# Kernel tuning notes

Measured on AMD Instinct MI355X. Metric: run time of the kernel, lower is better.

Reference implementation:

```python
import jax, jax.numpy as jnp
import numpy as np

VOCAB, ENC, EMB, DEC, ATT = 10000, 2048, 512, 512, 512
B, P, S = 64, 196, 20
PAD_ID = 0


def setup_inputs() -> dict:
    key = jax.random.key(0)
    ks = jax.random.split(key, 20)
    sc = lambda *sh: 1.0 / np.sqrt(sh[-1])
    def lin(k, out, inp):
        kw, kb = jax.random.split(k)
        s = 1.0 / np.sqrt(inp)
        return (jax.random.uniform(kw, (out, inp), jnp.float32, -s, s),
                jax.random.uniform(kb, (out,), jnp.float32, -s, s))
    wenc_w, wenc_b = lin(ks[0], ATT, ENC)
    wdec_w, wdec_b = lin(ks[1], ATT, DEC)
    V_w, V_b = lin(ks[2], 1, ATT)
    h0_w, h0_b = lin(ks[3], DEC, ENC)
    c0_w, c0_b = lin(ks[4], DEC, ENC)
    W_ih, b_ih = lin(ks[5], 4 * DEC, ENC + EMB)
    W_hh, b_hh = lin(ks[6], 4 * DEC, DEC)
    fc_w, fc_b = lin(ks[7], VOCAB, DEC)
    embed_w = jax.random.normal(ks[8], (VOCAB, EMB), jnp.float32)
    embed_w = embed_w.at[PAD_ID].set(0.0)  # padding_idx row is zero
    image_feat = jax.random.normal(ks[9], (B, P, ENC), jnp.float32)
    captions_ids = jax.random.randint(ks[10], (B, S), 0, VOCAB)
    return dict(image_feat=image_feat, captions_ids=captions_ids,
                wenc_w=wenc_w, wenc_b=wenc_b, wdec_w=wdec_w, wdec_b=wdec_b,
                V_w=V_w, V_b=V_b, embed_w=embed_w,
                h0_w=h0_w, h0_b=h0_b, c0_w=c0_w, c0_b=c0_b,
                W_ih=W_ih, b_ih=b_ih, W_hh=W_hh, b_hh=b_hh,
                fc_w=fc_w, fc_b=fc_b)


def reference(image_feat, captions_ids, wenc_w, wenc_b, wdec_w, wdec_b,
              V_w, V_b, embed_w, h0_w, h0_b, c0_w, c0_b,
              W_ih, b_ih, W_hh, b_hh, fc_w, fc_b):
    # eval mode: no input noise, dropout = identity
    avg = image_feat.mean(axis=1)                                   # [B, ENC]
    h = jax.nn.relu(avg @ h0_w.T + h0_b)                            # [B, DEC]
    c = jax.nn.relu(avg @ c0_w.T + c0_b)
    enc_proj = jnp.einsum('bpe,ae->bpa', image_feat, wenc_w) + wenc_b  # [B,P,ATT]
    emb_seq = embed_w[captions_ids]                                 # [B,S,EMB]
    emb_seq = jnp.transpose(emb_seq, (1, 0, 2))                     # [S,B,EMB]

    def step(carry, emb_t):
        h, c = carry
        att = jnp.tanh(enc_proj + (h @ wdec_w.T + wdec_b)[:, None, :])  # [B,P,ATT]
        e = jnp.einsum('bpa,a->bp', att, V_w[0]) + V_b[0]               # [B,P]
        w = jax.nn.softmax(e, axis=1)
        ctx = jnp.einsum('bp,bpe->be', w, image_feat)                   # [B,ENC]
        x = jnp.concatenate([ctx, emb_t], axis=1)                       # [B,ENC+EMB]
        gates = x @ W_ih.T + b_ih + h @ W_hh.T + b_hh                   # [B,4*DEC]
        i, f, g, o = jnp.split(gates, 4, axis=1)
        c_new = jax.nn.sigmoid(f) * c + jax.nn.sigmoid(i) * jnp.tanh(g)
        h_new = jax.nn.sigmoid(o) * jnp.tanh(c_new)
        logits = h_new @ fc_w.T + fc_b                                  # [B,VOCAB]
        return (h_new, c_new), logits

    _, preds = jax.lax.scan(step, (h, c), emb_seq)                  # [S,B,VOCAB]
    return jnp.transpose(preds, (1, 0, 2))                          # [B,S,VOCAB]
```

## Files before the change

kernel.cpp:

```cpp
#include <hip/hip_runtime.h>
#include <hip/hip_bf16.h>

#define DEV static __device__ __forceinline__

typedef short s16x8 __attribute__((ext_vector_type(8)));
typedef float f32x4 __attribute__((ext_vector_type(4)));
typedef unsigned short u16;

constexpr int Bn = 64, Pn = 196, ENCn = 2048, EMBn = 512, DECn = 512, ATTn = 512;
constexpr int VOCABn = 10000, Sn = 20;

DEV u16 f2bf(float x) {
  union { float f; unsigned u; } v; v.f = x;
  unsigned r = v.u + 0x7fffu + ((v.u >> 16) & 1u);
  return (u16)(r >> 16);
}
DEV float bf2f(u16 b) {
  union { unsigned u; float f; } v; v.u = ((unsigned)b) << 16;
  return v.f;
}
DEV float sigm(float x) { return 1.f / (1.f + __expf(-x)); }
DEV float tanh_fast(float x) {
  float e = __expf(2.f * x);
  return 1.f - 2.f / (e + 1.f);
}

DEV s16x8 ld8(const u16* p) { return *reinterpret_cast<const s16x8*>(p); }
DEV f32x4 mfma(s16x8 a, s16x8 b, f32x4 c) {
  return __builtin_amdgcn_mfma_f32_16x16x32_bf16(a, b, c, 0, 0, 0);
}

#define GLOAD_LDS16(gsrc, ldst)                                                \
  __builtin_amdgcn_global_load_lds(                                            \
      (const __attribute__((address_space(1))) void*)(gsrc),                   \
      (__attribute__((address_space(3))) void*)(ldst), 16, 0, 0)

__global__ __launch_bounds__(256) void k_cvtfeat_part(
    const float* __restrict__ feat, u16* __restrict__ featbf,
    float* __restrict__ pavg) {
  int b = blockIdx.y, px = blockIdx.x;
  int d8 = threadIdx.x * 8;
  const float* p = feat + ((size_t)b * Pn + px * 7) * ENCn + d8;
  u16* q = featbf + ((size_t)b * Pn + px * 7) * ENCn + d8;
  float acc[8] = {};
#pragma unroll
  for (int k = 0; k < 7; k++) {
    float4 v0 = *(const float4*)(p + (size_t)k * ENCn);
    float4 v1 = *(const float4*)(p + (size_t)k * ENCn + 4);
    acc[0] += v0.x; acc[1] += v0.y; acc[2] += v0.z; acc[3] += v0.w;
    acc[4] += v1.x; acc[5] += v1.y; acc[6] += v1.z; acc[7] += v1.w;
    s16x8 o;
    o[0] = (short)f2bf(v0.x); o[1] = (short)f2bf(v0.y);
    o[2] = (short)f2bf(v0.z); o[3] = (short)f2bf(v0.w);
    o[4] = (short)f2bf(v1.x); o[5] = (short)f2bf(v1.y);
    o[6] = (short)f2bf(v1.z); o[7] = (short)f2bf(v1.w);
    *(s16x8*)(q + (size_t)k * ENCn) = o;
  }
  float* pp = pavg + ((size_t)px * Bn + b) * ENCn + d8;
  *(f32x4*)pp = f32x4{acc[0], acc[1], acc[2], acc[3]};
  *(f32x4*)(pp + 4) = f32x4{acc[4], acc[5], acc[6], acc[7]};
}

__global__ __launch_bounds__(256) void k_avg_final(
    const float* __restrict__ pavg, float* __restrict__ avg) {
  int idx = blockIdx.x * 256 + threadIdx.x;
  int b = idx >> 9, e4 = (idx & 511) * 4;
  float4 s = {0.f, 0.f, 0.f, 0.f};
#pragma unroll
  for (int px = 0; px < 28; px++) {
    float4 v = *(const float4*)(pavg + ((size_t)px * Bn + b) * ENCn + e4);
    s.x += v.x; s.y += v.y; s.z += v.z; s.w += v.w;
  }
  float4 o = { s.x * (1.f/196.f), s.y * (1.f/196.f), s.z * (1.f/196.f), s.w * (1.f/196.f) };
  *(float4*)(avg + (size_t)b * ENCn + e4) = o;
}

__global__ void k_cvt_all(const float* __restrict__ s0, u16* __restrict__ d0,
                          const float* __restrict__ s1, u16* __restrict__ d1,
                          const float* __restrict__ s2, u16* __restrict__ d2,
                          const float* __restrict__ s3, u16* __restrict__ d3,
                          const float* __restrict__ s4, u16* __restrict__ d4,
                          const float* __restrict__ s5, u16* __restrict__ d5,
                          u16* __restrict__ wdecT) {
  int gid = blockIdx.x * 256 + threadIdx.x, stride = gridDim.x * 256;
  auto run = [&](const float* __restrict__ s, u16* __restrict__ d, int n8) {
    for (int i = gid; i < n8; i += stride) {
      const float4* sp = (const float4*)(s + (size_t)i * 8);
      float4 a = sp[0], b = sp[1];
      s16x8 o;
      o[0] = (short)f2bf(a.x); o[1] = (short)f2bf(a.y);
      o[2] = (short)f2bf(a.z); o[3] = (short)f2bf(a.w);
      o[4] = (short)f2bf(b.x); o[5] = (short)f2bf(b.y);
      o[6] = (short)f2bf(b.z); o[7] = (short)f2bf(b.w);
      *(s16x8*)(d + (size_t)i * 8) = o;
    }
  };
  run(s0, d0, 131072);
  run(s1, d1, 32768);
  run(s2, d2, 655360);
  run(s3, d3, 131072);
  run(s4, d4, 640000);
  run(s5, d5, 640000);
  for (int i = gid; i < 262144; i += stride) {
    int n = i >> 9, k = i & 511;
    wdecT[(size_t)k * 512 + n] = f2bf(s1[i]);
  }
}

__global__ __launch_bounds__(256) void k_h0c0(
    const float* __restrict__ avg,
    const float* __restrict__ h0w, const float* __restrict__ h0b,
    const float* __restrict__ c0w, const float* __restrict__ c0b,
    u16* __restrict__ h0out, float* __restrict__ c0out,
    float* __restrict__ decpart) {
  int idx = blockIdx.x * 256 + threadIdx.x;
  float* dz = decpart + (size_t)Bn * 512;
#pragma unroll
  for (int j = 0; j < 6; j++) dz[(size_t)j * 16384 + idx] = 0.f;

  int wid = threadIdx.x >> 6, lane = threadIdx.x & 63;
  int r = lane & 15, hi = lane >> 4;
  bool isC = blockIdx.x >= 32;
  int n0 = ((int)blockIdx.x & 31) * 16;
  const float* W = (isC ? c0w : h0w) + (size_t)(n0 + r) * ENCn + hi * 8;
  const float* ap = avg + (size_t)(wid * 16 + r) * ENCn + hi * 8;
  f32x4 acc = {0.f, 0.f, 0.f, 0.f};
  for (int k = 0; k < ENCn; k += 32) {
    s16x8 af, wf;
#pragma unroll
    for (int j = 0; j < 8; j++) { af[j] = (short)f2bf(ap[k + j]); wf[j] = (short)f2bf(W[k + j]); }
    acc = mfma(af, wf, acc);
  }
  int col = n0 + r;
  float bb = (isC ? c0b : h0b)[col];
#pragma unroll
  for (int j = 0; j < 4; j++) {
    int row = wid * 16 + hi * 4 + j;
    float v = fmaxf(acc[j] + bb, 0.f);
    if (isC) c0out[(size_t)row * DECn + col] = v;
    else     h0out[(size_t)row * DECn + col] = f2bf(v);
  }
}

template<typename TA, typename TW, int K>
__global__ __launch_bounds__(256) void k_lin64(
    const TA* __restrict__ A, const TW* __restrict__ W,
    const float* __restrict__ bias1, float* __restrict__ outF, size_t ldo) {
  int wid = threadIdx.x >> 6, lane = threadIdx.x & 63;
  int r = lane & 15, hi = lane >> 4;
  int n0 = blockIdx.x * 16;
  const TA* ap = A + (size_t)(wid * 16 + r) * K + hi * 8;
  const TW* wp = W + (size_t)(n0 + r) * K + hi * 8;
  f32x4 acc = {0.f, 0.f, 0.f, 0.f};
  for (int k = 0; k < K; k += 32) acc = mfma(ld8(ap + k), ld8(wp + k), acc);
  int col = n0 + r;
  float bb = bias1 ? bias1[col] : 0.f;
#pragma unroll
  for (int j = 0; j < 4; j++) {
    int row = wid * 16 + hi * 4 + j;
    outF[(size_t)row * ldo + col] = acc[j] + bb;
  }
}

__global__ __launch_bounds__(256) void k_bigproj(
    const u16* __restrict__ Abf, const u16* __restrict__ Wih,
    const u16* __restrict__ Wenc, const float* __restrict__ encb,
    u16* __restrict__ G, u16* __restrict__ encp) {
  __shared__ u16 As[128][32];
  __shared__ u16 Bs[128][32];
  int tid = threadIdx.x;
  int wid = tid >> 6, lane = tid & 63, r = lane & 15, hi = lane >> 4;
  int wm = wid >> 1, wn = wid & 1;
  int m0 = blockIdx.y * 128;
  bool isG = blockIdx.x < 16;
  int n0 = (isG ? (int)blockIdx.x : (int)blockIdx.x - 16) * 128;
  int srow = tid >> 2;
  int scol = (((tid & 3) ^ (srow & 3))) * 8;
  const u16* ga = Abf + (size_t)(m0 + srow) * ENCn + scol;
  const u16 *gb1, *gb2;
  if (isG) {
    int c1 = n0 + srow, c2 = n0 + 64 + srow;
    int w1 = (c1 >> 2) + (c1 & 3) * 512;
    int w2 = (c2 >> 2) + (c2 & 3) * 512;
    gb1 = Wih + (size_t)w1 * 2560 + scol;
    gb2 = Wih + (size_t)w2 * 2560 + scol;
  } else {
    gb1 = Wenc + (size_t)(n0 + srow) * ENCn + scol;
    gb2 = Wenc + (size_t)(n0 + 64 + srow) * ENCn + scol;
  }
  u16* As1 = &As[0][0];
  u16* Bs1 = &Bs[0][0];
  int sa = (hi ^ (r & 3)) * 8;
  f32x4 acc[4][4] = {};
  for (int k0 = 0; k0 < ENCn; k0 += 32) {
    GLOAD_LDS16(ga + k0,                      As1 + wid * 512);
    GLOAD_LDS16(ga + k0 + (size_t)64 * ENCn,  As1 + 2048 + wid * 512);
    GLOAD_LDS16(gb1 + k0,                     Bs1 + wid * 512);
    GLOAD_LDS16(gb2 + k0,                     Bs1 + 2048 + wid * 512);
    __syncthreads();
    s16x8 af[4], bfr[4];
#pragma unroll
    for (int i = 0; i < 4; i++) af[i]  = *(const s16x8*)(As1 + (wm * 64 + i * 16 + r) * 32 + sa);
#pragma unroll
    for (int j = 0; j < 4; j++) bfr[j] = *(const s16x8*)(Bs1 + (wn * 64 + j * 16 + r) * 32 + sa);
#pragma unroll
    for (int i = 0; i < 4; i++)
#pragma unroll
      for (int j = 0; j < 4; j++)
        acc[i][j] = mfma(af[i], bfr[j], acc[i][j]);
    __syncthreads();
  }
#pragma unroll
  for (int i = 0; i < 4; i++)
#pragma unroll
    for (int j = 0; j < 4; j++) {
      int col = n0 + wn * 64 + j * 16 + r;
#pragma unroll
      for (int q = 0; q < 4; q++) {
        int row = m0 + wm * 64 + i * 16 + hi * 4 + q;
        if (isG) G[(size_t)row * 2048 + col] = f2bf(acc[i][j][q]);
        else     encp[(size_t)row * 512 + col] = f2bf(acc[i][j][q] + encb[col]);
      }
    }
}

__global__ __launch_bounds__(256) void k_eproj(
    const u16* __restrict__ embbf, const int* __restrict__ caps,
    const u16* __restrict__ Wih, float* __restrict__ E) {
  __shared__ u16 As[128][32];
  __shared__ u16 Bs[128][32];
  int tid = threadIdx.x;
  int wid = tid >> 6, lane = tid & 63, r = lane & 15, hi = lane >> 4;
  int wm = wid >> 1, wn = wid & 1;
  int m0 = blockIdx.y * 128, n0 = blockIdx.x * 128;
  int srow = tid >> 2;
  int scol = (((tid & 3) ^ (srow & 3))) * 8;
  int row1 = m0 + srow, row2 = row1 + 64;
  int id1 = caps[(row1 & 63) * Sn + (row1 >> 6)];
  int id2 = caps[(row2 & 63) * Sn + (row2 >> 6)];
  const u16* ga1 = embbf + (size_t)id1 * 512 + scol;
  const u16* ga2 = embbf + (size_t)id2 * 512 + scol;
  const u16* gb1 = Wih + (size_t)(n0 + srow) * 2560 + 2048 + scol;
  const u16* gb2 = Wih + (size_t)(n0 + 64 + srow) * 2560 + 2048 + scol;
  u16* As1 = &As[0][0];
  u16* Bs1 = &Bs[0][0];
  int sa = (hi ^ (r & 3)) * 8;
  f32x4 acc[4][4] = {};
  for (int k0 = 0; k0 < 512; k0 += 32) {
    GLOAD_LDS16(ga1 + k0, As1 + wid * 512);
    GLOAD_LDS16(ga2 + k0, As1 + 2048 + wid * 512);
    GLOAD_LDS16(gb1 + k0, Bs1 + wid * 512);
    GLOAD_LDS16(gb2 + k0, Bs1 + 2048 + wid * 512);
    __syncthreads();
    s16x8 af[4], bfr[4];
#pragma unroll
    for (int i = 0; i < 4; i++) af[i]  = *(const s16x8*)(As1 + (wm * 64 + i * 16 + r) * 32 + sa);
#pragma unroll
    for (int j = 0; j < 4; j++) bfr[j] = *(const s16x8*)(Bs1 + (wn * 64 + j * 16 + r) * 32 + sa);
#pragma unroll
    for (int i = 0; i < 4; i++)
#pragma unroll
      for (int j = 0; j < 4; j++)
        acc[i][j] = mfma(af[i], bfr[j], acc[i][j]);
    __syncthreads();
  }
#pragma unroll
  for (int i = 0; i < 4; i++)
#pragma unroll
    for (int j = 0; j < 4; j++) {
      int col = n0 + wn * 64 + j * 16 + r;
#pragma unroll
      for (int q = 0; q < 4; q++) {
        int row = m0 + wm * 64 + i * 16 + hi * 4 + q;
        E[(size_t)row * 2048 + col] = acc[i][j][q];
      }
    }
}

__global__ __launch_bounds__(256) void k_step1(
    const u16* __restrict__ encp, const float* __restrict__ decpart,
    const float* __restrict__ wdecb,
    const float* __restrict__ Vw, const float* __restrict__ Vb,
    float* __restrict__ e_s,
    const u16* __restrict__ hin, const u16* __restrict__ Whh,
    float* __restrict__ p2) {
  int bx = blockIdx.x, by = blockIdx.y;
  int wid = threadIdx.x >> 6, lane = threadIdx.x & 63;
  if (bx < 49) {
    int p = bx * 4 + wid, b = by;
    int cb = lane * 8;
    float4 dv0 = *(const float4*)(wdecb + cb);
    float4 dv1 = *(const float4*)(wdecb + cb + 4);
#pragma unroll
    for (int q = 0; q < 4; q++) {
      const float* dq = decpart + ((size_t)q * Bn + b) * 512 + cb;
      float4 v0 = *(const float4*)dq, v1 = *(const float4*)(dq + 4);
      dv0.x += v0.x; dv0.y += v0.y; dv0.z += v0.z; dv0.w += v0.w;
      dv1.x += v1.x; dv1.y += v1.y; dv1.z += v1.z; dv1.w += v1.w;
    }
    float4 vv0 = *(const float4*)(Vw + cb), vv1 = *(const float4*)(Vw + cb + 4);
    s16x8 ev = *(const s16x8*)(encp + (((size_t)(b * Pn + p)) << 9) + cb);
    float s = 0.f;
    s += vv0.x * tanh_fast(bf2f((u16)ev[0]) + dv0.x);
    s += vv0.y * tanh_fast(bf2f((u16)ev[1]) + dv0.y);
    s += vv0.z * tanh_fast(bf2f((u16)ev[2]) + dv0.z);
    s += vv0.w * tanh_fast(bf2f((u16)ev[3]) + dv0.w);
    s += vv1.x * tanh_fast(bf2f((u16)ev[4]) + dv1.x);
    s += vv1.y * tanh_fast(bf2f((u16)ev[5]) + dv1.y);
    s += vv1.z * tanh_fast(bf2f((u16)ev[6]) + dv1.z);
    s += vv1.w * tanh_fast(bf2f((u16)ev[7]) + dv1.w);
    for (int m = 32; m; m >>= 1) s += __shfl_xor(s, m);
    if (lane == 0) e_s[(size_t)b * Pn + p] = s + Vb[0];
  } else {
    int sb = (bx - 49) * 64 + by;
    int n0 = sb * 16;
    int r = lane & 15, hi = lane >> 4;
    int brow = wid * 16 + r;
    f32x4 acc = {0.f, 0.f, 0.f, 0.f};
    const u16* a2 = hin + (size_t)brow * DECn + hi * 8;
    const u16* w2 = Whh + (size_t)(n0 + r) * 512 + hi * 8;
#pragma unroll 4
    for (int k = 0; k < 512; k += 32) acc = mfma(ld8(a2 + k), ld8(w2 + k), acc);
#pragma unroll
    for (int j = 0; j < 4; j++) {
      int row = wid * 16 + hi * 4 + j;
      p2[(size_t)row * 2048 + n0 + r] = acc[j];
    }
  }
}

__global__ __launch_bounds__(512) void k_step2(
    const float* __restrict__ e_s, const u16* __restrict__ G,
    const float* __restrict__ p2, const float* __restrict__ Et,
    const float* __restrict__ bih, const float* __restrict__ bhh,
    float* __restrict__ cbuf, u16* __restrict__ hnew,
    const u16* __restrict__ wdecT, float* __restrict__ decpart) {
  __shared__ float sw[Pn];
  __shared__ float red[512];
  __shared__ float pacc[8 * 512];
  __shared__ float hsh[128];
  int b = blockIdx.y, c = blockIdx.x, tid = threadIdx.x;
  float ev = (tid < Pn) ? e_s[(size_t)b * Pn + tid] : -3.0e38f;
  red[tid] = ev; __syncthreads();
  for (int s = 256; s > 0; s >>= 1) { if (tid < s) red[tid] = fmaxf(red[tid], red[tid + s]); __syncthreads(); }
  float m = red[0]; __syncthreads();
  float ex = (tid < Pn) ? __expf(ev - m) : 0.f;
  red[tid] = ex; __syncthreads();
  for (int s = 256; s > 0; s >>= 1) { if (tid < s) red[tid] += red[tid + s]; __syncthreads(); }
  float inv = 1.f / red[0];
  if (tid < Pn) sw[tid] = ex * inv;
  __syncthreads();
  int g = tid >> 6, t64 = tid & 63;
  int dloc = t64 * 8;
  const u16* gp = G + (size_t)b * Pn * 2048 + c * 512 + dloc;
  float acc[8] = {};
#pragma unroll 2
  for (int p = g; p < Pn; p += 8) {
    float w = sw[p];
    s16x8 v = *(const s16x8*)(gp + (size_t)p * 2048);
#pragma unroll
    for (int j = 0; j < 8; j++) acc[j] += w * bf2f((u16)v[j]);
  }
#pragma unroll
  for (int j = 0; j < 8; j++) pacc[g * 512 + j * 64 + t64] = acc[j];
  __syncthreads();
  if (tid < 128) {
    int d = c * 128 + tid;
    float gv[4];
#pragma unroll
    for (int gg = 0; gg < 4; gg++) {
      int lc = tid * 4 + gg;
      int ia = (lc & 7) * 64 + (lc >> 3);
      float s = 0.f;
#pragma unroll
      for (int gr = 0; gr < 8; gr++) s += pacc[gr * 512 + ia];
      int col = gg * 512 + d;
      gv[gg] = s + p2[(size_t)b * 2048 + col] + Et[(size_t)b * 2048 + col]
             + bih[col] + bhh[col];
    }
    size_t ci = (size_t)b * DECn + d;
    float cn = sigm(gv[1]) * cbuf[ci] + sigm(gv[0]) * tanh_fast(gv[2]);
    float hn = sigm(gv[3]) * tanh_fast(cn);
    cbuf[ci] = cn;
    hnew[ci] = f2bf(hn);
    hsh[tid] = hn;
  }
  __syncthreads();
  float a0 = 0.f;
#pragma unroll 8
  for (int k = 0; k < 128; k++)
    a0 += hsh[k] * bf2f(wdecT[(size_t)(c * 128 + k) * 512 + tid]);
  decpart[((size_t)c * Bn + b) * 512 + tid] = a0;
}

__global__ __launch_bounds__(256) void k_logits(
    const u16* __restrict__ hA, const u16* __restrict__ Wbf,
    const float* __restrict__ bias, float* __restrict__ out) {
  __shared__ u16 As[128][32];
  __shared__ u16 Bs[128][32];
  int tid = threadIdx.x;
  int wid = tid >> 6, lane = tid & 63, r = lane & 15, hi = lane >> 4;
  int wm = wid >> 1, wn = wid & 1;
  int m0 = blockIdx.y * 128, n0 = blockIdx.x * 128;
  int srow = tid >> 2;
  int scol = (((tid & 3) ^ (srow & 3))) * 8;
  const u16* ga = hA + (size_t)(m0 + srow) * 512 + scol;
  int br1 = n0 + srow;       if (br1 > VOCABn - 1) br1 = VOCABn - 1;
  int br2 = n0 + 64 + srow;  if (br2 > VOCABn - 1) br2 = VOCABn - 1;
  const u16* gb1 = Wbf + (size_t)br1 * 512 + scol;
  const u16* gb2 = Wbf + (size_t)br2 * 512 + scol;
  u16* As1 = &As[0][0];
  u16* Bs1 = &Bs[0][0];
  int sa = (hi ^ (r & 3)) * 8;
  f32x4 acc[4][4] = {};
  for (int k0 = 0; k0 < 512; k0 += 32) {
    GLOAD_LDS16(ga + k0,                     As1 + wid * 512);
    GLOAD_LDS16(ga + k0 + (size_t)64 * 512,  As1 + 2048 + wid * 512);
    GLOAD_LDS16(gb1 + k0,                    Bs1 + wid * 512);
    GLOAD_LDS16(gb2 + k0,                    Bs1 + 2048 + wid * 512);
    __syncthreads();
    s16x8 af[4], bfr[4];
#pragma unroll
    for (int i = 0; i < 4; i++) af[i]  = *(const s16x8*)(As1 + (wm * 64 + i * 16 + r) * 32 + sa);
#pragma unroll
    for (int j = 0; j < 4; j++) bfr[j] = *(const s16x8*)(Bs1 + (wn * 64 + j * 16 + r) * 32 + sa);
#pragma unroll
    for (int i = 0; i < 4; i++)
#pragma unroll
      for (int j = 0; j < 4; j++)
        acc[i][j] = mfma(af[i], bfr[j], acc[i][j]);
    __syncthreads();
  }
#pragma unroll
  for (int i = 0; i < 4; i++)
#pragma unroll
    for (int j = 0; j < 4; j++) {
      int col = n0 + wn * 64 + j * 16 + r;
      if (col < VOCABn) {
        float bb = bias[col];
#pragma unroll
        for (int q = 0; q < 4; q++) {
          int row = m0 + wm * 64 + i * 16 + hi * 4 + q;
          int tt = row >> 6, b = row & 63;
          out[((size_t)b * Sn + tt) * VOCABn + col] = acc[i][j][q] + bb;
        }
      }
    }
}

extern "C" void kernel_launch(void* const* d_in, const int* in_sizes, int n_in,
                              void* d_out, int out_size, void* d_ws, size_t ws_size,
                              hipStream_t stream) {
  const float* image_feat = (const float*)d_in[0];
  const int*   captions   = (const int*)d_in[1];
  const float* wenc_w = (const float*)d_in[2];
  const float* wenc_b = (const float*)d_in[3];
  const float* wdec_w = (const float*)d_in[4];
  const float* wdec_b = (const float*)d_in[5];
  const float* V_w    = (const float*)d_in[6];
  const float* V_b    = (const float*)d_in[7];
  const float* embed_w = (const float*)d_in[8];
  const float* h0_w = (const float*)d_in[9];
  const float* h0_b = (const float*)d_in[10];
  const float* c0_w = (const float*)d_in[11];
  const float* c0_b = (const float*)d_in[12];
  const float* W_ih = (const float*)d_in[13];
  const float* b_ih = (const float*)d_in[14];
  const float* W_hh = (const float*)d_in[15];
  const float* b_hh = (const float*)d_in[16];
  const float* fc_w = (const float*)d_in[17];
  const float* fc_b = (const float*)d_in[18];
  float* out = (float*)d_out;

  char* w = (char*)d_ws;
  auto alloc = [&](size_t bytes) { void* p = (void*)w; w += (bytes + 255) & ~(size_t)255; return p; };
  u16* if_bf   = (u16*)alloc(sizeof(u16) * (size_t)Bn * Pn * ENCn);
  u16* Gbuf    = (u16*)alloc(sizeof(u16) * (size_t)Bn * Pn * 2048);
  u16* wenc_bf = (u16*)alloc(sizeof(u16) * (size_t)ATTn * ENCn);
  u16* wdec_bf = (u16*)alloc(sizeof(u16) * (size_t)ATTn * DECn);
  u16* wdecT   = (u16*)alloc(sizeof(u16) * (size_t)DECn * DECn);
  u16* Wih_bf  = (u16*)alloc(sizeof(u16) * (size_t)2048 * 2560);
  u16* Whh_bf  = (u16*)alloc(sizeof(u16) * (size_t)2048 * 512);
  u16* fcw_bf  = (u16*)alloc(sizeof(u16) * (size_t)VOCABn * DECn);
  u16* emb_bf  = (u16*)alloc(sizeof(u16) * (size_t)VOCABn * EMBn);
  u16* hall    = (u16*)alloc(sizeof(u16) * (size_t)(Sn + 1) * Bn * DECn);
  u16* encp    = (u16*)alloc(sizeof(u16) * (size_t)Bn * Pn * ATTn);
  float* Ebuf  = (float*)alloc(sizeof(float) * (size_t)Sn * Bn * 2048);
  float* avg   = (float*)alloc(sizeof(float) * (size_t)Bn * ENCn);
  float* pavg  = (float*)alloc(sizeof(float) * (size_t)28 * Bn * ENCn);
  float* e_s   = (float*)alloc(sizeof(float) * (size_t)Bn * Pn);
  float* cbuf  = (float*)alloc(sizeof(float) * (size_t)Bn * DECn);
  float* p2    = (float*)alloc(sizeof(float) * (size_t)Bn * 2048);
  float* decpart = (float*)alloc(sizeof(float) * (size_t)4 * Bn * 512);

  k_cvtfeat_part<<<dim3(28, Bn), 256, 0, stream>>>(image_feat, if_bf, pavg);
  k_avg_final<<<128, 256, 0, stream>>>(pavg, avg);
  k_cvt_all<<<2048, 256, 0, stream>>>(wenc_w, wenc_bf, wdec_w, wdec_bf,
                                      W_ih, Wih_bf, W_hh, Whh_bf, fc_w, fcw_bf,
                                      embed_w, emb_bf, wdecT);
  k_bigproj<<<dim3(20, 98), 256, 0, stream>>>(if_bf, Wih_bf, wenc_bf, wenc_b,
                                              Gbuf, encp);
  k_eproj<<<dim3(16, 10), 256, 0, stream>>>(emb_bf, captions, Wih_bf, Ebuf);
  k_h0c0<<<64, 256, 0, stream>>>(avg, h0_w, h0_b, c0_w, c0_b, hall, cbuf, decpart);
  k_lin64<u16, u16, 512><<<32, 256, 0, stream>>>(hall, wdec_bf, nullptr, decpart, 512);

  for (int t = 0; t < Sn; t++) {
    const u16* hin = hall + (size_t)t * Bn * DECn;
    u16* hnew = hall + (size_t)(t + 1) * Bn * DECn;
    k_step1<<<dim3(51, Bn), 256, 0, stream>>>(encp, decpart, wdec_b, V_w, V_b, e_s,
                                              hin, Whh_bf, p2);
    k_step2<<<dim3(4, Bn), 512, 0, stream>>>(e_s, Gbuf, p2,
                                             Ebuf + (size_t)t * Bn * 2048,
                                             b_ih, b_hh, cbuf, hnew, wdecT, decpart);
  }
  k_logits<<<dim3(79, 10), 256, 0, stream>>>(hall + (size_t)Bn * DECn, fcw_bf, fc_b, out);
}
```

Baseline: 990.2 us.

## Fold avg reduction into weight conversion kernel and drop LDS XOR swizzle

Moves the final per-pixel-group average reduction into the tail of the bulk weight conversion kernel, removing one kernel launch. It also removes the XOR swizzle on LDS column offsets in the three MFMA GEMM kernels, making the store and load offsets plain. Dropping the swizzle makes the address math simpler but can bring back LDS bank conflicts on the fragment reads, since each row is only 64 bytes wide.

```diff
diff --git a/kernel.cpp b/kernel.cpp
--- a/kernel.cpp
+++ b/kernel.cpp
@@ -61,27 +61,14 @@
   *(f32x4*)(pp + 4) = f32x4{acc[4], acc[5], acc[6], acc[7]};
 }
 
-__global__ __launch_bounds__(256) void k_avg_final(
-    const float* __restrict__ pavg, float* __restrict__ avg) {
-  int idx = blockIdx.x * 256 + threadIdx.x;
-  int b = idx >> 9, e4 = (idx & 511) * 4;
-  float4 s = {0.f, 0.f, 0.f, 0.f};
-#pragma unroll
-  for (int px = 0; px < 28; px++) {
-    float4 v = *(const float4*)(pavg + ((size_t)px * Bn + b) * ENCn + e4);
-    s.x += v.x; s.y += v.y; s.z += v.z; s.w += v.w;
-  }
-  float4 o = { s.x * (1.f/196.f), s.y * (1.f/196.f), s.z * (1.f/196.f), s.w * (1.f/196.f) };
-  *(float4*)(avg + (size_t)b * ENCn + e4) = o;
-}
-
 __global__ void k_cvt_all(const float* __restrict__ s0, u16* __restrict__ d0,
                           const float* __restrict__ s1, u16* __restrict__ d1,
                           const float* __restrict__ s2, u16* __restrict__ d2,
                           const float* __restrict__ s3, u16* __restrict__ d3,
                           const float* __restrict__ s4, u16* __restrict__ d4,
                           const float* __restrict__ s5, u16* __restrict__ d5,
-                          u16* __restrict__ wdecT) {
+                          u16* __restrict__ wdecT,
+                          const float* __restrict__ pavg, float* __restrict__ avg) {
   int gid = blockIdx.x * 256 + threadIdx.x, stride = gridDim.x * 256;
   auto run = [&](const float* __restrict__ s, u16* __restrict__ d, int n8) {
     for (int i = gid; i < n8; i += stride) {
@@ -104,6 +91,17 @@
   for (int i = gid; i < 262144; i += stride) {
     int n = i >> 9, k = i & 511;
     wdecT[(size_t)k * 512 + n] = f2bf(s1[i]);
+  }
+  for (int i = gid; i < 32768; i += stride) {
+    int b = i >> 9, e4 = (i & 511) * 4;
+    float4 s = {0.f, 0.f, 0.f, 0.f};
+#pragma unroll
+    for (int px = 0; px < 28; px++) {
+      float4 v = *(const float4*)(pavg + ((size_t)px * Bn + b) * ENCn + e4);
+      s.x += v.x; s.y += v.y; s.z += v.z; s.w += v.w;
+    }
+    float4 o = { s.x * (1.f/196.f), s.y * (1.f/196.f), s.z * (1.f/196.f), s.w * (1.f/196.f) };
+    *(float4*)(avg + (size_t)b * ENCn + e4) = o;
   }
 }
 
@@ -174,8 +172,7 @@
   int m0 = blockIdx.y * 128;
   bool isG = blockIdx.x < 16;
   int n0 = (isG ? (int)blockIdx.x : (int)blockIdx.x - 16) * 128;
-  int srow = tid >> 2;
-  int scol = (((tid & 3) ^ (srow & 3))) * 8;
+  int srow = tid >> 2, scol = (tid & 3) * 8;
   const u16* ga = Abf + (size_t)(m0 + srow) * ENCn + scol;
   const u16 *gb1, *gb2;
   if (isG) {
@@ -190,7 +187,6 @@
   }
   u16* As1 = &As[0][0];
   u16* Bs1 = &Bs[0][0];
-  int sa = (hi ^ (r & 3)) * 8;
   f32x4 acc[4][4] = {};
   for (int k0 = 0; k0 < ENCn; k0 += 32) {
     GLOAD_LDS16(ga + k0,                      As1 + wid * 512);
@@ -200,9 +196,9 @@
     __syncthreads();
     s16x8 af[4], bfr[4];
 #pragma unroll
-    for (int i = 0; i < 4; i++) af[i]  = *(const s16x8*)(As1 + (wm * 64 + i * 16 + r) * 32 + sa);
-#pragma unroll
-    for (int j = 0; j < 4; j++) bfr[j] = *(const s16x8*)(Bs1 + (wn * 64 + j * 16 + r) * 32 + sa);
+    for (int i = 0; i < 4; i++) af[i]  = *(const s16x8*)(As1 + (wm * 64 + i * 16 + r) * 32 + hi * 8);
+#pragma unroll
+    for (int j = 0; j < 4; j++) bfr[j] = *(const s16x8*)(Bs1 + (wn * 64 + j * 16 + r) * 32 + hi * 8);
 #pragma unroll
     for (int i = 0; i < 4; i++)
 #pragma unroll
@@ -233,8 +229,7 @@
   int wid = tid >> 6, lane = tid & 63, r = lane & 15, hi = lane >> 4;
   int wm = wid >> 1, wn = wid & 1;
   int m0 = blockIdx.y * 128, n0 = blockIdx.x * 128;
-  int srow = tid >> 2;
-  int scol = (((tid & 3) ^ (srow & 3))) * 8;
+  int srow = tid >> 2, scol = (tid & 3) * 8;
   int row1 = m0 + srow, row2 = row1 + 64;
   int id1 = caps[(row1 & 63) * Sn + (row1 >> 6)];
   int id2 = caps[(row2 & 63) * Sn + (row2 >> 6)];
@@ -244,7 +239,6 @@
   const u16* gb2 = Wih + (size_t)(n0 + 64 + srow) * 2560 + 2048 + scol;
   u16* As1 = &As[0][0];
   u16* Bs1 = &Bs[0][0];
-  int sa = (hi ^ (r & 3)) * 8;
   f32x4 acc[4][4] = {};
   for (int k0 = 0; k0 < 512; k0 += 32) {
     GLOAD_LDS16(ga1 + k0, As1 + wid * 512);
@@ -254,9 +248,9 @@
     __syncthreads();
     s16x8 af[4], bfr[4];
 #pragma unroll
-    for (int i = 0; i < 4; i++) af[i]  = *(const s16x8*)(As1 + (wm * 64 + i * 16 + r) * 32 + sa);
-#pragma unroll
-    for (int j = 0; j < 4; j++) bfr[j] = *(const s16x8*)(Bs1 + (wn * 64 + j * 16 + r) * 32 + sa);
+    for (int i = 0; i < 4; i++) af[i]  = *(const s16x8*)(As1 + (wm * 64 + i * 16 + r) * 32 + hi * 8);
+#pragma unroll
+    for (int j = 0; j < 4; j++) bfr[j] = *(const s16x8*)(Bs1 + (wn * 64 + j * 16 + r) * 32 + hi * 8);
 #pragma unroll
     for (int i = 0; i < 4; i++)
 #pragma unroll
@@ -402,8 +396,7 @@
   int wid = tid >> 6, lane = tid & 63, r = lane & 15, hi = lane >> 4;
   int wm = wid >> 1, wn = wid & 1;
   int m0 = blockIdx.y * 128, n0 = blockIdx.x * 128;
-  int srow = tid >> 2;
-  int scol = (((tid & 3) ^ (srow & 3))) * 8;
+  int srow = tid >> 2, scol = (tid & 3) * 8;
   const u16* ga = hA + (size_t)(m0 + srow) * 512 + scol;
   int br1 = n0 + srow;       if (br1 > VOCABn - 1) br1 = VOCABn - 1;
   int br2 = n0 + 64 + srow;  if (br2 > VOCABn - 1) br2 = VOCABn - 1;
@@ -411,7 +404,6 @@
   const u16* gb2 = Wbf + (size_t)br2 * 512 + scol;
   u16* As1 = &As[0][0];
   u16* Bs1 = &Bs[0][0];
-  int sa = (hi ^ (r & 3)) * 8;
   f32x4 acc[4][4] = {};
   for (int k0 = 0; k0 < 512; k0 += 32) {
     GLOAD_LDS16(ga + k0,                     As1 + wid * 512);
@@ -421,9 +413,9 @@
     __syncthreads();
     s16x8 af[4], bfr[4];
 #pragma unroll
-    for (int i = 0; i < 4; i++) af[i]  = *(const s16x8*)(As1 + (wm * 64 + i * 16 + r) * 32 + sa);
-#pragma unroll
-    for (int j = 0; j < 4; j++) bfr[j] = *(const s16x8*)(Bs1 + (wn * 64 + j * 16 + r) * 32 + sa);
+    for (int i = 0; i < 4; i++) af[i]  = *(const s16x8*)(As1 + (wm * 64 + i * 16 + r) * 32 + hi * 8);
+#pragma unroll
+    for (int j = 0; j < 4; j++) bfr[j] = *(const s16x8*)(Bs1 + (wn * 64 + j * 16 + r) * 32 + hi * 8);
 #pragma unroll
     for (int i = 0; i < 4; i++)
 #pragma unroll
@@ -494,10 +486,9 @@
   float* decpart = (float*)alloc(sizeof(float) * (size_t)4 * Bn * 512);
 
   k_cvtfeat_part<<<dim3(28, Bn), 256, 0, stream>>>(image_feat, if_bf, pavg);
-  k_avg_final<<<128, 256, 0, stream>>>(pavg, avg);
   k_cvt_all<<<2048, 256, 0, stream>>>(wenc_w, wenc_bf, wdec_w, wdec_bf,
                                       W_ih, Wih_bf, W_hh, Whh_bf, fc_w, fcw_bf,
-                                      embed_w, emb_bf, wdecT);
+                                      embed_w, emb_bf, wdecT, pavg, avg);
   k_bigproj<<<dim3(20, 98), 256, 0, stream>>>(if_bf, Wih_bf, wenc_bf, wenc_b,
                                               Gbuf, encp);
   k_eproj<<<dim3(16, 10), 256, 0, stream>>>(emb_bf, captions, Wih_bf, Ebuf);
```

New measurement: 990.2 us. About the same (-0.0%).
